# Kernel optimization log

Hardware: AMD Instinct MI355X
Metric: run time of the kernel (lower is better)

Reference implementation:

```python
import jax, jax.numpy as jnp
import numpy as np


def _lstm(x, h0, c0, Wih, Whh, b):
    """Single-layer LSTM, batch_first input x: [B,T,D]. PyTorch gate order i,f,g,o.
    Returns (h_seq [T,B,H], h_T [B,H], c_T [B,H])."""
    xs = jnp.swapaxes(x, 0, 1)  # [T,B,D]

    def step(carry, xt):
        h, c = carry
        gates = xt @ Wih.T + h @ Whh.T + b  # [B,4H]
        i, f, g, o = jnp.split(gates, 4, axis=-1)
        c = jax.nn.sigmoid(f) * c + jax.nn.sigmoid(i) * jnp.tanh(g)
        h = jax.nn.sigmoid(o) * jnp.tanh(c)
        return (h, c), h

    (h, c), hs = jax.lax.scan(step, (h0, c0), xs)
    return hs, h, c


def setup_inputs() -> dict:
    key = jax.random.key(0)
    ks = jax.random.split(key, 16)
    B, T, Tf, Tu = 256, 365, 15, 76
    Dh, Df, Du, H = 64, 32, 16, 256
    s = 1.0 / np.sqrt(H)  # torch-style uniform scale, approximated with scaled normals
    return {
        "x_d": jax.random.normal(ks[0], (B, T, Dh), jnp.float32),
        "x_f": jax.random.normal(ks[1], (B, Tf, Df), jnp.float32),
        "x_ff": jax.random.normal(ks[2], (B, Tu, Du), jnp.float32),
        "enc_Wih": jax.random.normal(ks[3], (4 * H, Dh), jnp.float32) * s,
        "enc_Whh": jax.random.normal(ks[4], (4 * H, H), jnp.float32) * s,
        "enc_b": jax.random.normal(ks[5], (4 * H,), jnp.float32) * s,
        "decf_Wih": jax.random.normal(ks[6], (4 * H, Df), jnp.float32) * s,
        "decf_Whh": jax.random.normal(ks[7], (4 * H, H), jnp.float32) * s,
        "decf_b": jax.random.normal(ks[8], (4 * H,), jnp.float32) * s,
        "decu_Wih": jax.random.normal(ks[9], (4 * H, Du), jnp.float32) * s,
        "decu_Whh": jax.random.normal(ks[10], (4 * H, H), jnp.float32) * s,
        "decu_b": jax.random.normal(ks[11], (4 * H,), jnp.float32) * s,
        "head_W": jax.random.normal(ks[12], (1, H), jnp.float32) * s,
        "head_b": jax.random.normal(ks[13], (1,), jnp.float32) * s,
    }


def reference(x_d, x_f, x_ff, enc_Wih, enc_Whh, enc_b,
              decf_Wih, decf_Whh, decf_b, decu_Wih, decu_Whh, decu_b,
              head_W, head_b):
    B = x_d.shape[0]
    H = enc_Whh.shape[1]
    Tf = x_f.shape[1]
    Tu = x_ff.shape[1]
    horizon = Tf + Tu
    h0 = jnp.zeros((B, H), x_d.dtype)
    c0 = jnp.zeros((B, H), x_d.dtype)

    # Encoder over historical sequence
    _, h, c = _lstm(x_d, h0, c0, enc_Wih, enc_Whh, enc_b)

    # Forecast decoder: one LSTM step per horizon step + linear head (dropout = eval identity)
    hs_f, h, c = _lstm(x_f, h, c, decf_Wih, decf_Whh, decf_b)  # [Tf,B,H]
    out_f = (jnp.einsum('tbh,oh->tbo', hs_f, head_W)[..., 0] + head_b[0]).T  # [B,Tf]

    # Future decoder, continuing the hidden state
    hs_u, h, c = _lstm(x_ff, h, c, decu_Wih, decu_Whh, decu_b)  # [Tu,B,H]
    out_u = (jnp.einsum('tbh,oh->tbo', hs_u, head_W)[..., 0] + head_b[0]).T  # [B,Tu]

    # Faithful to original: both loops write outputs[:, t], so the future loop
    # overwrites the first Tu columns.
    outputs = jnp.zeros((B, horizon), x_d.dtype)
    outputs = outputs.at[:, :Tf].set(out_f)
    outputs = outputs.at[:, :Tu].set(out_u)
    return outputs
```

## Files before the change

### kernel.cpp

```cpp
#include <hip/hip_runtime.h>
#include <stdint.h>


typedef __attribute__((ext_vector_type(8))) short short8;
typedef __attribute__((ext_vector_type(4))) float f32x4;
typedef __attribute__((ext_vector_type(2))) unsigned int u32x2;

#define L2E 1.4426950408889634f

__device__ __forceinline__ uint16_t f2bf(float f) {
  uint32_t x = __float_as_uint(f);
  x += 0x7fffu + ((x >> 16) & 1u);
  return (uint16_t)(x >> 16);
}
__device__ __forceinline__ uint32_t pk2(float a, float b) {
  return (uint32_t)f2bf(a) | ((uint32_t)f2bf(b) << 16);
}
__device__ __forceinline__ uint32_t cvtpk(float lo, float hi) {
  uint32_t r;
  asm("v_cvt_pk_bf16_f32 %0, %1, %2" : "=v"(r) : "v"(lo), "v"(hi));
  return r;
}
__device__ __forceinline__ float bfhalf(uint32_t w, int hi) {
  return __uint_as_float(hi ? (w & 0xffff0000u) : (w << 16));
}
__device__ __forceinline__ f32x4 MFMA(short8 a, short8 b, f32x4 c) {
  return __builtin_amdgcn_mfma_f32_16x16x32_bf16(a, b, c, 0, 0, 0);
}
__device__ __forceinline__ float ex2(float x) { return __builtin_amdgcn_exp2f(x); }
__device__ __forceinline__ float rcp(float x) { return __builtin_amdgcn_rcpf(x); }

__device__ __forceinline__ void lgkm_barrier() {
  __builtin_amdgcn_sched_barrier(0);
  asm volatile("s_waitcnt lgkmcnt(0)" ::: "memory");
  __builtin_amdgcn_s_barrier();
  __builtin_amdgcn_sched_barrier(0);
}
__device__ __forceinline__ void vm_drain4() {
  __builtin_amdgcn_sched_barrier(0);
  asm volatile("s_waitcnt vmcnt(4)" ::: "memory");
  __builtin_amdgcn_sched_barrier(0);
}

__global__ void init_kernel(float* c_state, uint16_t* h_state, float* out,
                            uint32_t* flags) {
  int i = blockIdx.x * 256 + threadIdx.x;
  if (i < 65536) { c_state[i] = 0.f; h_state[i] = 0; }
  if (i < 256 * 91) out[i] = 0.f;
  if (i < 96) flags[i] = 0;
}

template <int DIN>
__global__ __launch_bounds__(512) void xproj_kernel(
    const float* __restrict__ x, const float* __restrict__ Wih,
    const float* __restrict__ bias, uint32_t* __restrict__ xp,
    int t0, int T) {
  const int tid = threadIdx.x, w = tid >> 6, l = tid & 63;
  const int l16 = l & 15, lg = l >> 4;
  const int tc = blockIdx.x >> 1;
  const int sub = blockIdx.x & 1;
  const int t = t0 + tc;
  constexpr int KT = (DIN + 31) / 32;

  short8 bfr[8][KT];
  float4 bias4[8];
#pragma unroll
  for (int ni = 0; ni < 8; ++ni) {
    const int n = (w * 8 + ni) * 16 + l16;
    bias4[ni] = *(const float4*)&bias[(w * 8 + ni) * 16 + lg * 4];
#pragma unroll
    for (int kt = 0; kt < KT; ++kt) {
      const int k0 = kt * 32 + lg * 8;
      short8 fr;
#pragma unroll
      for (int e = 0; e < 8; ++e) fr[e] = 0;
      if (k0 + 8 <= DIN) {
        const float* s = Wih + (size_t)n * DIN + k0;
#pragma unroll
        for (int e = 0; e < 8; ++e) fr[e] = (short)f2bf(s[e]);
      }
      bfr[ni][kt] = fr;
    }
  }

  for (int mi = 0; mi < 8; ++mi) {
    const int btile = sub * 8 + mi;
    const int b = btile * 16 + l16;
    short8 af[KT];
#pragma unroll
    for (int kt = 0; kt < KT; ++kt) {
      const int k0 = kt * 32 + lg * 8;
      short8 fr;
#pragma unroll
      for (int e = 0; e < 8; ++e) fr[e] = 0;
      if (k0 + 8 <= DIN) {
        const float* s = x + ((size_t)b * T + t) * DIN + k0;
#pragma unroll
        for (int e = 0; e < 8; ++e) fr[e] = (short)f2bf(s[e]);
      }
      af[kt] = fr;
    }
#pragma unroll
    for (int ni = 0; ni < 8; ++ni) {
      f32x4 acc = {0.f, 0.f, 0.f, 0.f};
#pragma unroll
      for (int kt = 0; kt < KT; ++kt) acc = MFMA(bfr[ni][kt], af[kt], acc);
      const int nt = w * 8 + ni;
      const float sc = ((nt >> 4) == 2) ? (2.f * L2E) : -L2E;
      size_t idx = ((((size_t)tc * 16 + btile) * 64 + nt) * 64 + l) * 2;
      u32x2 v;
      v[0] = pk2((acc[0] + bias4[ni].x) * sc, (acc[1] + bias4[ni].y) * sc);
      v[1] = pk2((acc[2] + bias4[ni].z) * sc, (acc[3] + bias4[ni].w) * sc);
      *(u32x2*)(xp + idx) = v;
    }
  }
}

template <int DO_HEAD>
__global__ __launch_bounds__(512, 2) void rec_kernel(
    const uint32_t* __restrict__ xp, const float* __restrict__ Whh,
    float* __restrict__ c_state, uint16_t* __restrict__ h_state,
    float* __restrict__ out, const float* __restrict__ headW,
    const float* __restrict__ headb, uint32_t* __restrict__ flags,
    unsigned long long* __restrict__ hx, uint32_t* __restrict__ hxh,
    int ct, int t0, int phase) {
  __shared__ short8 B_lds[64 * 64];
  __shared__ uint16_t h_lds[2][16][264];
  __shared__ float headbuf[16][8];

  const int tid = threadIdx.x, w = tid >> 6, l = tid & 63;
  const int l16 = l & 15, lg = l >> 4;
  const int blk = blockIdx.x;
  const int pair = blk & 15, s = blk >> 4, sp = 1 - s;
  const int b0 = pair * 16;
  const int ctile = s * 8 + w;
  uint32_t* const pflag = flags + (phase * 16 + pair) * 2 + sp;
  uint32_t* const myflag = flags + (phase * 16 + pair) * 2 + s;

  short8 bv[24];
#pragma unroll
  for (int g = 0; g < 4; ++g) {
    const float wsc = (g == 2) ? (2.f * L2E) : -L2E;
#pragma unroll
    for (int kt = 0; kt < 8; ++kt) {
      const int row = (g * 16 + ctile) * 16 + l16;
      const float* sw = Whh + (size_t)row * 256 + kt * 32 + lg * 8;
      short8 fr;
#pragma unroll
      for (int e = 0; e < 8; ++e) fr[e] = (short)f2bf(sw[e] * wsc);
      if (kt <= 5) bv[g * 6 + kt] = fr;
      else B_lds[(w * 8 + g * 2 + (kt - 6)) * 64 + l] = fr;
    }
  }

  float c_reg[4];
  {
    float4 c4 = *(const float4*)&c_state[(size_t)(b0 + l16) * 256 +
                                         ctile * 16 + lg * 4];
    c_reg[0] = c4.x; c_reg[1] = c4.y; c_reg[2] = c4.z; c_reg[3] = c4.w;
  }
  for (int idx = tid; idx < 16 * 256; idx += 512)
    h_lds[0][idx >> 8][idx & 255] = h_state[(size_t)(b0 + (idx >> 8)) * 256 + (idx & 255)];
  float4 hw4 = *(const float4*)&headW[ctile * 16 + lg * 4];
  const float hb = headb[0];

  const uint32_t* xpb = xp + ((size_t)(pair * 64 + ctile) * 64 + l) * 2;
  u32x2 xpf[4];
#pragma unroll
  for (int g = 0; g < 4; ++g)
    xpf[g] = *(const u32x2*)(xpb + (size_t)g * 2048);

  __syncthreads();

  for (int t = 0; t < ct; ++t) {
    const int cur = t & 1, nxt = cur ^ 1;
    const int tn = (t + 1 < ct) ? t + 1 : t;
    const int par = t & 1;
    const uint32_t tgt = (uint32_t)(t0 + t + 1);
    float hsum = 0.f;

    f32x4 acc[4];
#pragma unroll
    for (int g = 0; g < 4; ++g) {
      f32x4 ai;
      ai[0] = bfhalf(xpf[g][0], 0);
      ai[1] = bfhalf(xpf[g][0], 1);
      ai[2] = bfhalf(xpf[g][1], 0);
      ai[3] = bfhalf(xpf[g][1], 1);
      acc[g] = ai;
    }
#pragma unroll
    for (int kt = 0; kt < 8; ++kt) {
      short8 hf = *(const short8*)(&h_lds[cur][l16][kt * 32 + lg * 8]);
#pragma unroll
      for (int g = 0; g < 4; ++g) {
        if (kt <= 5) acc[g] = MFMA(bv[g * 6 + kt], hf, acc[g]);
        else acc[g] = MFMA(B_lds[(w * 8 + g * 2 + (kt - 6)) * 64 + l], hf, acc[g]);
      }
    }

    float hv[4];
#pragma unroll
    for (int j = 0; j < 4; ++j) {
      float ei = ex2(acc[0][j]);
      float ef = ex2(acc[1][j]);
      float eg = ex2(acc[2][j]);
      float eo = ex2(acc[3][j]);
      float eip = 1.f + ei, egp = eg + 1.f, efp = 1.f + ef;
      float d1 = eip * egp;
      float R = rcp(d1 * efp);
      float sitg = (eg - 1.f) * efp * R;
      float cc = fmaf(c_reg[j] * d1, R, sitg);
      c_reg[j] = cc;
      float ec = ex2(cc * (2.f * L2E));
      float hh = (ec - 1.f) * rcp((1.f + eo) * (ec + 1.f));
      hv[j] = hh;
    }

    u32x2 hwrd;
    hwrd[0] = cvtpk(hv[0], hv[1]);
    hwrd[1] = cvtpk(hv[2], hv[3]);
    *(u32x2*)(&h_lds[nxt][l16][ctile * 16 + lg * 4]) = hwrd;
    {
      unsigned long long v64 =
          ((unsigned long long)hwrd[1] << 32) | (unsigned long long)hwrd[0];
      unsigned long long* dst =
          hx + ((size_t)((pair * 2 + s) * 2 + par) * 512) + (w * 4 + lg) * 16 + l16;
      __hip_atomic_store(dst, v64, __ATOMIC_RELAXED, __HIP_MEMORY_SCOPE_AGENT);
    }

#pragma unroll
    for (int g = 0; g < 4; ++g)
      xpf[g] = *(const u32x2*)(xpb + (size_t)tn * 131072 + g * 2048);

    if (DO_HEAD) {
      float hp = fmaf(hv[0], hw4.x, fmaf(hv[1], hw4.y,
                 fmaf(hv[2], hw4.z, hv[3] * hw4.w)));
      hp += __shfl_xor(hp, 16);
      hp += __shfl_xor(hp, 32);
      if (lg == 0) headbuf[l16][w] = hp;
    }

    vm_drain4();
    lgkm_barrier();

    if (DO_HEAD) {
      if (tid < 16) {
        const float* hbp = headbuf[tid];
        hsum = hbp[0] + hbp[1] + hbp[2] + hbp[3] +
               hbp[4] + hbp[5] + hbp[6] + hbp[7];
        __hip_atomic_store(hxh + ((pair * 2 + s) * 2 + par) * 16 + tid,
                           __float_as_uint(hsum), __ATOMIC_RELAXED,
                           __HIP_MEMORY_SCOPE_AGENT);
      }
      vm_drain4();
    }
    if (tid == 0)
      __hip_atomic_store(myflag, tgt, __ATOMIC_RELAXED, __HIP_MEMORY_SCOPE_AGENT);

    __builtin_amdgcn_sched_barrier(0);
    uint32_t f;
    do {
      f = __hip_atomic_load(pflag, __ATOMIC_RELAXED, __HIP_MEMORY_SCOPE_AGENT);
    } while ((int)(f - tgt) < 0);
    __builtin_amdgcn_sched_barrier(0);

    {
      const unsigned long long* src =
          hx + ((size_t)((pair * 2 + sp) * 2 + par) * 512) + (w * 4 + lg) * 16 + l16;
      unsigned long long pv =
          __hip_atomic_load(src, __ATOMIC_RELAXED, __HIP_MEMORY_SCOPE_AGENT);
      u32x2 pw;
      pw[0] = (uint32_t)pv;
      pw[1] = (uint32_t)(pv >> 32);
      *(u32x2*)(&h_lds[nxt][l16][sp * 128 + w * 16 + lg * 4]) = pw;
    }
    if (DO_HEAD && s == 0) {
      if (tid < 16) {
        uint32_t pp = __hip_atomic_load(
            hxh + ((pair * 2 + sp) * 2 + par) * 16 + tid,
            __ATOMIC_RELAXED, __HIP_MEMORY_SCOPE_AGENT);
        out[(size_t)(b0 + tid) * 91 + (t0 + t)] = hsum + __uint_as_float(pp) + hb;
      }
    }

    lgkm_barrier();
  }

  {
    float4 c4 = {c_reg[0], c_reg[1], c_reg[2], c_reg[3]};
    *(float4*)&c_state[(size_t)(b0 + l16) * 256 + ctile * 16 + lg * 4] = c4;
  }
  if (s == 0)
    for (int idx = tid; idx < 16 * 256; idx += 512)
      h_state[(size_t)(b0 + (idx >> 8)) * 256 + (idx & 255)] =
          h_lds[ct & 1][idx >> 8][idx & 255];
}

extern "C" void kernel_launch(void* const* d_in, const int* in_sizes, int n_in,
                              void* d_out, int out_size, void* d_ws, size_t ws_size,
                              hipStream_t stream) {
  const float* headW = (const float*)d_in[12];
  const float* headb = (const float*)d_in[13];
  float* out = (float*)d_out;

  char* ws = (char*)d_ws;
  float* c_state = (float*)ws;
  uint16_t* h_state = (uint16_t*)(ws + 262144);
  uint32_t* flags = (uint32_t*)(ws + 393216);
  unsigned long long* hx = (unsigned long long*)(ws + 397312);
  uint32_t* hxh = (uint32_t*)(ws + 659456);
  uint32_t* xp = (uint32_t*)(ws + 667648);

  int ct_max = 1;
  if (ws_size > 667648 + 512 * 1024) {
    size_t c = (ws_size - 667648) / (512 * 1024);
    ct_max = (c > 365) ? 365 : (int)c;
  }

  init_kernel<<<256, 256, 0, stream>>>(c_state, h_state, out, flags);

  struct Phase { const float* x; const float* Wih; const float* Whh; const float* b; int T; int D; int head; };
  Phase ph[3] = {
      {(const float*)d_in[0], (const float*)d_in[3], (const float*)d_in[4], (const float*)d_in[5],
       in_sizes[0] / (256 * 64), 64, 0},
      {(const float*)d_in[1], (const float*)d_in[6], (const float*)d_in[7], (const float*)d_in[8],
       in_sizes[1] / (256 * 32), 32, 0},
      {(const float*)d_in[2], (const float*)d_in[9], (const float*)d_in[10], (const float*)d_in[11],
       in_sizes[2] / (256 * 16), 16, 1},
  };

  for (int pi = 0; pi < 3; ++pi) {
    const Phase& P = ph[pi];
    for (int t0 = 0; t0 < P.T; t0 += ct_max) {
      int ct = (P.T - t0 < ct_max) ? (P.T - t0) : ct_max;
      dim3 g(ct * 2);
      if (P.D == 64)
        xproj_kernel<64><<<g, 512, 0, stream>>>(P.x, P.Wih, P.b, xp, t0, P.T);
      else if (P.D == 32)
        xproj_kernel<32><<<g, 512, 0, stream>>>(P.x, P.Wih, P.b, xp, t0, P.T);
      else
        xproj_kernel<16><<<g, 512, 0, stream>>>(P.x, P.Wih, P.b, xp, t0, P.T);
      if (P.head)
        rec_kernel<1><<<32, 512, 0, stream>>>(xp, P.Whh, c_state, h_state, out,
                                              headW, headb, flags, hx, hxh,
                                              ct, t0, pi);
      else
        rec_kernel<0><<<32, 512, 0, stream>>>(xp, P.Whh, c_state, h_state, out,
                                              headW, headb, flags, hx, hxh,
                                              ct, t0, pi);
    }
  }
}
```

Before: 1.298 ms.

## Overlap partner hidden-state exchange with local-half MFMA in LSTM step

Each block of a pair now starts the recurrent matmul on the half of h it produced itself and only waits for the partner block's flag afterwards. It then merges the partner's half into LDS and finishes the remaining K tiles. The Whh fragments are reordered so the local K tiles come first, and the head output write and final state writeback move to after the wait. This hides the cross-block flag latency behind half of the MFMA work, at the cost of an extra LDS barrier mid-step and more complex end-of-loop handling.

```diff
diff --git a/kernel.cpp b/kernel.cpp
--- a/kernel.cpp
+++ b/kernel.cpp
@@ -142,14 +142,15 @@
   for (int g = 0; g < 4; ++g) {
     const float wsc = (g == 2) ? (2.f * L2E) : -L2E;
 #pragma unroll
-    for (int kt = 0; kt < 8; ++kt) {
+    for (int kk = 0; kk < 8; ++kk) {
+      const int kt = (kk < 4) ? (4 * s + kk) : (4 * sp + (kk - 4));
       const int row = (g * 16 + ctile) * 16 + l16;
       const float* sw = Whh + (size_t)row * 256 + kt * 32 + lg * 8;
       short8 fr;
 #pragma unroll
       for (int e = 0; e < 8; ++e) fr[e] = (short)f2bf(sw[e] * wsc);
-      if (kt <= 5) bv[g * 6 + kt] = fr;
-      else B_lds[(w * 8 + g * 2 + (kt - 6)) * 64 + l] = fr;
+      if (kk <= 5) bv[g * 6 + kk] = fr;
+      else B_lds[(w * 8 + g * 2 + (kk - 6)) * 64 + l] = fr;
     }
   }
 
@@ -172,12 +173,36 @@
 
   __syncthreads();
 
+  u32x2 h_last;
+  h_last[0] = 0; h_last[1] = 0;
+  float hsum_prev = 0.f;
+
   for (int t = 0; t < ct; ++t) {
     const int cur = t & 1, nxt = cur ^ 1;
     const int tn = (t + 1 < ct) ? t + 1 : t;
     const int par = t & 1;
-    const uint32_t tgt = (uint32_t)(t0 + t + 1);
-    float hsum = 0.f;
+
+    unsigned long long pv = 0ull;
+    if (t > 0) {
+      const uint32_t tgt = (uint32_t)(t0 + t);
+      __builtin_amdgcn_sched_barrier(0);
+      uint32_t f;
+      do {
+        f = __hip_atomic_load(pflag, __ATOMIC_RELAXED, __HIP_MEMORY_SCOPE_AGENT);
+      } while ((int)(f - tgt) < 0);
+      __builtin_amdgcn_sched_barrier(0);
+      pv = __hip_atomic_load(
+          hx + ((size_t)((pair * 2 + sp) * 2 + ((t - 1) & 1)) * 512) +
+              (w * 4 + lg) * 16 + l16,
+          __ATOMIC_RELAXED, __HIP_MEMORY_SCOPE_AGENT);
+      if (DO_HEAD && s == 0 && tid < 16) {
+        uint32_t pp = __hip_atomic_load(
+            hxh + ((pair * 2 + sp) * 2 + ((t - 1) & 1)) * 16 + tid,
+            __ATOMIC_RELAXED, __HIP_MEMORY_SCOPE_AGENT);
+        out[(size_t)(b0 + tid) * 91 + (t0 + t - 1)] =
+            hsum_prev + __uint_as_float(pp) + hb;
+      }
+    }
 
     f32x4 acc[4];
 #pragma unroll
@@ -190,12 +215,28 @@
       acc[g] = ai;
     }
 #pragma unroll
-    for (int kt = 0; kt < 8; ++kt) {
-      short8 hf = *(const short8*)(&h_lds[cur][l16][kt * 32 + lg * 8]);
+    for (int kk = 0; kk < 4; ++kk) {
+      short8 hf = *(const short8*)(&h_lds[cur][l16][(4 * s + kk) * 32 + lg * 8]);
+#pragma unroll
+      for (int g = 0; g < 4; ++g)
+        acc[g] = MFMA(bv[g * 6 + kk], hf, acc[g]);
+    }
+
+    if (t > 0) {
+      u32x2 pw;
+      pw[0] = (uint32_t)pv;
+      pw[1] = (uint32_t)(pv >> 32);
+      *(u32x2*)(&h_lds[cur][l16][sp * 128 + w * 16 + lg * 4]) = pw;
+      lgkm_barrier();
+    }
+
+#pragma unroll
+    for (int kk = 0; kk < 4; ++kk) {
+      short8 hf = *(const short8*)(&h_lds[cur][l16][(4 * sp + kk) * 32 + lg * 8]);
 #pragma unroll
       for (int g = 0; g < 4; ++g) {
-        if (kt <= 5) acc[g] = MFMA(bv[g * 6 + kt], hf, acc[g]);
-        else acc[g] = MFMA(B_lds[(w * 8 + g * 2 + (kt - 6)) * 64 + l], hf, acc[g]);
+        if (kk < 2) acc[g] = MFMA(bv[g * 6 + 4 + kk], hf, acc[g]);
+        else acc[g] = MFMA(B_lds[(w * 8 + g * 2 + (kk - 2)) * 64 + l], hf, acc[g]);
       }
     }
 
@@ -217,16 +258,15 @@
       hv[j] = hh;
     }
 
-    u32x2 hwrd;
-    hwrd[0] = cvtpk(hv[0], hv[1]);
-    hwrd[1] = cvtpk(hv[2], hv[3]);
-    *(u32x2*)(&h_lds[nxt][l16][ctile * 16 + lg * 4]) = hwrd;
+    h_last[0] = cvtpk(hv[0], hv[1]);
+    h_last[1] = cvtpk(hv[2], hv[3]);
+    *(u32x2*)(&h_lds[nxt][l16][ctile * 16 + lg * 4]) = h_last;
     {
       unsigned long long v64 =
-          ((unsigned long long)hwrd[1] << 32) | (unsigned long long)hwrd[0];
-      unsigned long long* dst =
-          hx + ((size_t)((pair * 2 + s) * 2 + par) * 512) + (w * 4 + lg) * 16 + l16;
-      __hip_atomic_store(dst, v64, __ATOMIC_RELAXED, __HIP_MEMORY_SCOPE_AGENT);
+          ((unsigned long long)h_last[1] << 32) | (unsigned long long)h_last[0];
+      __hip_atomic_store(
+          hx + ((size_t)((pair * 2 + s) * 2 + par) * 512) + (w * 4 + lg) * 16 + l16,
+          v64, __ATOMIC_RELAXED, __HIP_MEMORY_SCOPE_AGENT);
     }
 
 #pragma unroll
@@ -247,54 +287,49 @@
     if (DO_HEAD) {
       if (tid < 16) {
         const float* hbp = headbuf[tid];
-        hsum = hbp[0] + hbp[1] + hbp[2] + hbp[3] +
-               hbp[4] + hbp[5] + hbp[6] + hbp[7];
+        hsum_prev = hbp[0] + hbp[1] + hbp[2] + hbp[3] +
+                    hbp[4] + hbp[5] + hbp[6] + hbp[7];
         __hip_atomic_store(hxh + ((pair * 2 + s) * 2 + par) * 16 + tid,
-                           __float_as_uint(hsum), __ATOMIC_RELAXED,
+                           __float_as_uint(hsum_prev), __ATOMIC_RELAXED,
                            __HIP_MEMORY_SCOPE_AGENT);
       }
       vm_drain4();
     }
     if (tid == 0)
-      __hip_atomic_store(myflag, tgt, __ATOMIC_RELAXED, __HIP_MEMORY_SCOPE_AGENT);
-
+      __hip_atomic_store(myflag, (uint32_t)(t0 + t + 1), __ATOMIC_RELAXED,
+                         __HIP_MEMORY_SCOPE_AGENT);
+  }
+
+  {
+    float4 c4 = {c_reg[0], c_reg[1], c_reg[2], c_reg[3]};
+    *(float4*)&c_state[(size_t)(b0 + l16) * 256 + ctile * 16 + lg * 4] = c4;
+  }
+
+  if (s == 0) {
+    const uint32_t tgt = (uint32_t)(t0 + ct);
     __builtin_amdgcn_sched_barrier(0);
     uint32_t f;
     do {
       f = __hip_atomic_load(pflag, __ATOMIC_RELAXED, __HIP_MEMORY_SCOPE_AGENT);
     } while ((int)(f - tgt) < 0);
     __builtin_amdgcn_sched_barrier(0);
-
-    {
-      const unsigned long long* src =
-          hx + ((size_t)((pair * 2 + sp) * 2 + par) * 512) + (w * 4 + lg) * 16 + l16;
-      unsigned long long pv =
-          __hip_atomic_load(src, __ATOMIC_RELAXED, __HIP_MEMORY_SCOPE_AGENT);
-      u32x2 pw;
-      pw[0] = (uint32_t)pv;
-      pw[1] = (uint32_t)(pv >> 32);
-      *(u32x2*)(&h_lds[nxt][l16][sp * 128 + w * 16 + lg * 4]) = pw;
-    }
-    if (DO_HEAD && s == 0) {
-      if (tid < 16) {
-        uint32_t pp = __hip_atomic_load(
-            hxh + ((pair * 2 + sp) * 2 + par) * 16 + tid,
-            __ATOMIC_RELAXED, __HIP_MEMORY_SCOPE_AGENT);
-        out[(size_t)(b0 + tid) * 91 + (t0 + t)] = hsum + __uint_as_float(pp) + hb;
-      }
-    }
-
-    lgkm_barrier();
-  }
-
-  {
-    float4 c4 = {c_reg[0], c_reg[1], c_reg[2], c_reg[3]};
-    *(float4*)&c_state[(size_t)(b0 + l16) * 256 + ctile * 16 + lg * 4] = c4;
-  }
-  if (s == 0)
-    for (int idx = tid; idx < 16 * 256; idx += 512)
-      h_state[(size_t)(b0 + (idx >> 8)) * 256 + (idx & 255)] =
-          h_lds[ct & 1][idx >> 8][idx & 255];
+    unsigned long long pv = __hip_atomic_load(
+        hx + ((size_t)((pair * 2 + sp) * 2 + ((ct - 1) & 1)) * 512) +
+            (w * 4 + lg) * 16 + l16,
+        __ATOMIC_RELAXED, __HIP_MEMORY_SCOPE_AGENT);
+    u32x2 pw;
+    pw[0] = (uint32_t)pv;
+    pw[1] = (uint32_t)(pv >> 32);
+    *(u32x2*)&h_state[(size_t)(b0 + l16) * 256 + 128 + w * 16 + lg * 4] = pw;
+    *(u32x2*)&h_state[(size_t)(b0 + l16) * 256 + w * 16 + lg * 4] = h_last;
+    if (DO_HEAD && tid < 16) {
+      uint32_t pp = __hip_atomic_load(
+          hxh + ((pair * 2 + sp) * 2 + ((ct - 1) & 1)) * 16 + tid,
+          __ATOMIC_RELAXED, __HIP_MEMORY_SCOPE_AGENT);
+      out[(size_t)(b0 + tid) * 91 + (t0 + ct - 1)] =
+          hsum_prev + __uint_as_float(pp) + hb;
+    }
+  }
 }
 
 extern "C" void kernel_launch(void* const* d_in, const int* in_sizes, int n_in,
```

Result: faster. 1.248 ms (-3.9%).
